# Kernel optimization log

Hardware: AMD Instinct MI355X
Metric: run time of the kernel (lower is better)

The kernel has to match this reference:

```python
import jax, jax.numpy as jnp
import numpy as np

# dims: L=tgt len, S=src len, N=batch, E=embed, H=heads
L, S, N, E, H = 1024, 1024, 4, 1024, 16
HD = E // H  # head dim = 64


def setup_inputs() -> dict:
    key = jax.random.key(0)
    ks = jax.random.split(key, 7)
    w_scale = 0.02
    return {
        "query": jax.random.normal(ks[0], (L, N, E), jnp.float32),
        "key": jax.random.normal(ks[1], (S, N, E), jnp.float32),
        "value": jax.random.normal(ks[2], (S, N, E), jnp.float32),
        "in_proj_weight": jax.random.normal(ks[3], (3 * E, E), jnp.float32) * w_scale,
        "in_proj_bias": jax.random.normal(ks[4], (3 * E,), jnp.float32) * w_scale,
        "out_proj_weight": jax.random.normal(ks[5], (E, E), jnp.float32) * w_scale,
        "out_proj_bias": jax.random.normal(ks[6], (E,), jnp.float32) * w_scale,
    }


def reference(query, key, value, in_proj_weight, in_proj_bias,
              out_proj_weight, out_proj_bias):
    scaling = float(HD) ** -0.5
    # packed QKV projection, sliced exactly as the torch code does
    q = (query @ in_proj_weight[:E].T + in_proj_bias[:E]) * scaling        # (L,N,E)
    k = key @ in_proj_weight[E:2 * E].T + in_proj_bias[E:2 * E]            # (S,N,E)
    v = value @ in_proj_weight[2 * E:].T + in_proj_bias[2 * E:]            # (S,N,E)
    # split heads: (L,N,E) -> (N*H, L, HD)
    q = q.reshape(L, N * H, HD).transpose(1, 0, 2)
    k = k.reshape(S, N * H, HD).transpose(1, 0, 2)
    v = v.reshape(S, N * H, HD).transpose(1, 0, 2)
    scores = jnp.einsum('bld,bsd->bls', q, k)          # (N*H, L, S)
    attn = jax.nn.softmax(scores, axis=-1)
    sig = jax.nn.sigmoid(scores)                        # the need_sigmoid_weights variant
    out = jnp.einsum('bls,bsd->bld', attn, v)          # (N*H, L, HD)
    out = out.transpose(1, 0, 2).reshape(L, N, E)
    out = out @ out_proj_weight.T + out_proj_bias       # (L,N,E)
    # weights averaged over heads, as torch MHA returns: (N,L,S)
    attn_weights = attn.reshape(N, H, L, S).sum(axis=1) / H
    sig_weights = sig.reshape(N, H, L, S).sum(axis=1) / H
    return out, attn_weights, sig_weights
```

## Files before the change

kernel.cpp:

```cpp
#include <hip/hip_runtime.h>

#define L_DIM 1024
#define E_DIM 1024
#define NB 4
#define H_NUM 16
#define HD_DIM 64
#define T_TOK 4096
#define NHB 64

typedef float f32x4 __attribute__((ext_vector_type(4)));
typedef unsigned short u16x8 __attribute__((ext_vector_type(8)));
typedef unsigned short u16x4 __attribute__((ext_vector_type(4)));
typedef __bf16 bf16x8 __attribute__((ext_vector_type(8)));

__device__ inline unsigned short f2bf(float f) {
  unsigned int u = __builtin_bit_cast(unsigned int, f);
  u += 0x7FFFu + ((u >> 16) & 1u);
  return (unsigned short)(u >> 16);
}
__device__ __forceinline__ unsigned int cvt_pk_bf16(float lo, float hi) {
  unsigned int r;
  asm("v_cvt_pk_bf16_f32 %0, %1, %2" : "=v"(r) : "v"(lo), "v"(hi));
  return r;
}
__device__ inline f32x4 mfma16(u16x8 a, u16x8 b, f32x4 c) {
  return __builtin_amdgcn_mfma_f32_16x16x32_bf16(
      __builtin_bit_cast(bf16x8, a), __builtin_bit_cast(bf16x8, b), c, 0, 0, 0);
}

__device__ __forceinline__ void gl2lds16(const void* g, void* l) {
  auto gp = reinterpret_cast<const __attribute__((address_space(1))) unsigned int*>(
      reinterpret_cast<unsigned long long>(g));
  auto lp = reinterpret_cast<__attribute__((address_space(3))) unsigned int*>(
      static_cast<unsigned int>(reinterpret_cast<unsigned long long>(l)));
  __builtin_amdgcn_global_load_lds(gp, lp, 16, 0, 0);
}

__global__ __launch_bounds__(256) void cast_kernel(
    const float* __restrict__ s0, const float* __restrict__ s1,
    const float* __restrict__ s2, const float* __restrict__ s3,
    unsigned short* __restrict__ d0, unsigned short* __restrict__ d1,
    unsigned short* __restrict__ d2, unsigned short* __restrict__ d3,
    int n0, int n1, int n2, int n3) {
  const int y = blockIdx.y;
  const float* s = (y == 0) ? s0 : (y == 1) ? s1 : (y == 2) ? s2 : s3;
  unsigned short* d = (y == 0) ? d0 : (y == 1) ? d1 : (y == 2) ? d2 : d3;
  const int n = (y == 0) ? n0 : (y == 1) ? n1 : (y == 2) ? n2 : n3;
  int idx = (blockIdx.x * 256 + threadIdx.x) * 8;
  const int stride = gridDim.x * 256 * 8;
  for (; idx < n; idx += stride) {
    float4 a = *(const float4*)(s + idx);
    float4 b = *(const float4*)(s + idx + 4);
    u16x8 o = {f2bf(a.x), f2bf(a.y), f2bf(a.z), f2bf(a.w),
               f2bf(b.x), f2bf(b.y), f2bf(b.z), f2bf(b.w)};
    *(u16x8*)(d + idx) = o;
  }
}

__device__ __forceinline__ void stage_tile(const unsigned short* __restrict__ g,
                                           unsigned short* lbuf, int tid) {
  const int r = tid >> 2, c = tid & 3;
  const int sc = c ^ ((r ^ (r >> 2)) & 3);
  gl2lds16(g + (size_t)r * 1024 + sc * 8, lbuf + tid * 8);
  const int r2 = r + 64;
  gl2lds16(g + (size_t)r2 * 1024 + sc * 8, lbuf + (tid + 256) * 8);
}
__device__ __forceinline__ int frag_off(int r, int q) {
  return r * 32 + ((q ^ ((r ^ (r >> 2)) & 3)) << 3);
}

__global__ __launch_bounds__(256) void qkv_gemm(
    const unsigned short* __restrict__ qb, const unsigned short* __restrict__ kb,
    const unsigned short* __restrict__ vb, const unsigned short* __restrict__ Wb,
    const float* __restrict__ bias, unsigned short* __restrict__ q_hm,
    unsigned short* __restrict__ k_hm, unsigned short* __restrict__ v_t) {
  __shared__ __align__(16) unsigned short As[3][4096];
  __shared__ __align__(16) unsigned short Bs[3][4096];
  const int tid = threadIdx.x;
  const int bm = blockIdx.x, bn = blockIdx.y, z = blockIdx.z;
  const unsigned short* Ag = ((z == 0) ? qb : (z == 1) ? kb : vb) + (size_t)bm * 128 * 1024;
  const unsigned short* Bg = Wb + (size_t)z * 1048576 + (size_t)bn * 128 * 1024;
  const float* bc = bias + z * E_DIM;

  const int w = tid >> 6, lane = tid & 63;
  const int wm = w & 1, wn = w >> 1;
  const int quad = lane >> 4, l16 = lane & 15;

  f32x4 acc[4][4];
#pragma unroll
  for (int i = 0; i < 4; i++)
#pragma unroll
    for (int j = 0; j < 4; j++) { f32x4 zz = {0.f, 0.f, 0.f, 0.f}; acc[i][j] = zz; }

  stage_tile(Ag, As[0], tid);
  stage_tile(Bg, Bs[0], tid);

  int cb = 0, sb = 1;
#pragma unroll 1
  for (int kk = 0; kk < 32; kk++) {
    if (kk + 1 < 32) {
      stage_tile(Ag + (kk + 1) * 32, As[sb], tid);
      stage_tile(Bg + (kk + 1) * 32, Bs[sb], tid);
      sb = (sb == 2) ? 0 : sb + 1;
      asm volatile("s_waitcnt vmcnt(4)" ::: "memory");
    } else {
      asm volatile("s_waitcnt vmcnt(0)" ::: "memory");
    }
    __builtin_amdgcn_s_barrier();
    asm volatile("" ::: "memory");
    u16x8 af[4], bfv[4];
#pragma unroll
    for (int mi = 0; mi < 4; mi++) {
      int r = wm * 64 + mi * 16 + l16;
      af[mi] = *(const u16x8*)&As[cb][frag_off(r, quad)];
    }
#pragma unroll
    for (int ni = 0; ni < 4; ni++) {
      int r = wn * 64 + ni * 16 + l16;
      bfv[ni] = *(const u16x8*)&Bs[cb][frag_off(r, quad)];
    }
#pragma unroll
    for (int mi = 0; mi < 4; mi++)
#pragma unroll
      for (int ni = 0; ni < 4; ni++)
        acc[mi][ni] = mfma16(af[mi], bfv[ni], acc[mi][ni]);
    cb = (cb == 2) ? 0 : cb + 1;
  }
#pragma unroll
  for (int ni = 0; ni < 4; ni++) {
    int col = bn * 128 + wn * 64 + ni * 16 + l16;
    float bv = bc[col];
    int h = col >> 6, d = col & 63;
#pragma unroll
    for (int mi = 0; mi < 4; mi++) {
#pragma unroll
      for (int r = 0; r < 4; r++) {
        int t = bm * 128 + wm * 64 + mi * 16 + quad * 4 + r;
        float v = acc[mi][ni][r] + bv;
        int nb = t & 3, pos = t >> 2;
        if (z == 0) {
          v *= 0.125f;
          q_hm[(size_t)((nb * 16 + h) * 1024 + pos) * 64 + d] = f2bf(v);
        } else if (z == 1) {
          k_hm[(size_t)((nb * 16 + h) * 1024 + pos) * 64 + d] = f2bf(v);
        } else {
          v_t[(size_t)((nb * 16 + h) * 64 + d) * 1024 + pos] = f2bf(v);
        }
      }
    }
  }
}

__global__ __launch_bounds__(256, 2) void attn_kernel(
    const unsigned short* __restrict__ q_hm, const unsigned short* __restrict__ k_hm,
    const unsigned short* __restrict__ v_t, unsigned short* __restrict__ o_h,
    float* __restrict__ m_ws, float* __restrict__ r_ws) {
  __shared__ __align__(16) unsigned short stage[6][4096];
  __shared__ __align__(16) unsigned short pt[4][32][68];
  __shared__ float red_m[4][32];
  __shared__ float red_s[4][32];

  const int tid = threadIdx.x;
  const int flat = blockIdx.x + (blockIdx.y << 5);
  const int nf = (flat & 7) * 256 + (flat >> 3);
  const int l0 = (nf & 31) * 32;
  const int b = nf >> 5;
  const int nb = b >> 4, h = b & 15;
  const int w = tid >> 6, lane = tid & 63;
  const int quad = lane >> 4, l16 = lane & 15;

  const int i1 = tid + 256;
  const int r0s = tid >> 3, c0s = tid & 7;
  const int r1s = i1 >> 3, c1s = i1 & 7;
  const int src0 = (c0s ^ (r0s & 7)) * 8;
  const int src1 = (c1s ^ (r1s & 7)) * 8;

  const unsigned short* kbase = k_hm + ((size_t)b << 16);
  const unsigned short* vbase = v_t + ((size_t)b << 16);

  u16x8 bq[2][2];
#pragma unroll
  for (int g = 0; g < 2; g++) {
    const unsigned short* qp =
        q_hm + ((size_t)(b * 1024 + l0 + g * 16 + l16) << 6) + quad * 8;
    bq[g][0] = *(const u16x8*)qp;
    bq[g][1] = *(const u16x8*)(qp + 32);
  }
  asm volatile("" ::: "memory");

  f32x4 acc[16][2];
#pragma unroll
  for (int j = 0; j < 16; j++)
#pragma unroll
    for (int g = 0; g < 2; g++) { f32x4 z = {0.f, 0.f, 0.f, 0.f}; acc[j][g] = z; }

#pragma unroll
  for (int t = 0; t < 4; t++) {
    gl2lds16(kbase + ((size_t)(t * 64 + r0s) << 6) + src0, &stage[t][tid * 8]);
    gl2lds16(kbase + ((size_t)(t * 64 + r1s) << 6) + src1, &stage[t][i1 * 8]);
  }

  const int myrow = w * 16 + l16;
  const int sw0 = ((quad ^ (l16 & 7)) * 8);
  const int sw1 = (((quad + 4) ^ (l16 & 7)) * 8);

#pragma unroll
  for (int i = 0; i < 8; i++) {
    if (i >= 1) {
      const int t0 = 2 * i + 2, t1 = 2 * i + 3;
      if (t0 < 16) {
        gl2lds16(kbase + ((size_t)(t0 * 64 + r0s) << 6) + src0, &stage[t0 % 6][tid * 8]);
        gl2lds16(kbase + ((size_t)(t0 * 64 + r1s) << 6) + src1, &stage[t0 % 6][i1 * 8]);
        gl2lds16(kbase + ((size_t)(t1 * 64 + r0s) << 6) + src0, &stage[t1 % 6][tid * 8]);
        gl2lds16(kbase + ((size_t)(t1 * 64 + r1s) << 6) + src1, &stage[t1 % 6][i1 * 8]);
      } else {
        const int v0 = t0 - 16, v1 = t1 - 16;
        gl2lds16(vbase + ((size_t)r0s << 10) + v0 * 64 + src0, &stage[t0 % 6][tid * 8]);
        gl2lds16(vbase + ((size_t)r1s << 10) + v0 * 64 + src1, &stage[t0 % 6][i1 * 8]);
        gl2lds16(vbase + ((size_t)r0s << 10) + v1 * 64 + src0, &stage[t1 % 6][tid * 8]);
        gl2lds16(vbase + ((size_t)r1s << 10) + v1 * 64 + src1, &stage[t1 % 6][i1 * 8]);
      }
    }
    asm volatile("s_waitcnt vmcnt(4)" ::: "memory");
    __builtin_amdgcn_s_barrier();
    asm volatile("" ::: "memory");
    const int c0 = 2 * i, c1 = 2 * i + 1;
    const unsigned short* kt0 = &stage[c0 % 6][myrow * 64];
    const unsigned short* kt1 = &stage[c1 % 6][myrow * 64];
    u16x8 a00 = *(const u16x8*)(kt0 + sw0);
    u16x8 a01 = *(const u16x8*)(kt0 + sw1);
    u16x8 a10 = *(const u16x8*)(kt1 + sw0);
    u16x8 a11 = *(const u16x8*)(kt1 + sw1);
    acc[c0][0] = mfma16(a00, bq[0][0], acc[c0][0]);
    acc[c0][0] = mfma16(a01, bq[0][1], acc[c0][0]);
    acc[c0][1] = mfma16(a00, bq[1][0], acc[c0][1]);
    acc[c0][1] = mfma16(a01, bq[1][1], acc[c0][1]);
    acc[c1][0] = mfma16(a10, bq[0][0], acc[c1][0]);
    acc[c1][0] = mfma16(a11, bq[0][1], acc[c1][0]);
    acc[c1][1] = mfma16(a10, bq[1][0], acc[c1][1]);
    acc[c1][1] = mfma16(a11, bq[1][1], acc[c1][1]);
  }

  gl2lds16(vbase + ((size_t)r0s << 10) + 2 * 64 + src0, &stage[0][tid * 8]);
  gl2lds16(vbase + ((size_t)r1s << 10) + 2 * 64 + src1, &stage[0][i1 * 8]);
  gl2lds16(vbase + ((size_t)r0s << 10) + 3 * 64 + src0, &stage[1][tid * 8]);
  gl2lds16(vbase + ((size_t)r1s << 10) + 3 * 64 + src1, &stage[1][i1 * 8]);

  float lm0 = -3e38f, lm1 = -3e38f;
#pragma unroll
  for (int j = 0; j < 16; j++)
#pragma unroll
    for (int r = 0; r < 4; r++) {
      lm0 = fmaxf(lm0, acc[j][0][r]);
      lm1 = fmaxf(lm1, acc[j][1][r]);
    }
  lm0 = fmaxf(lm0, __shfl_xor(lm0, 16, 64));
  lm0 = fmaxf(lm0, __shfl_xor(lm0, 32, 64));
  lm1 = fmaxf(lm1, __shfl_xor(lm1, 16, 64));
  lm1 = fmaxf(lm1, __shfl_xor(lm1, 32, 64));
  if (lane < 16) { red_m[w][lane] = lm0; red_m[w][lane + 16] = lm1; }
  asm volatile("s_waitcnt lgkmcnt(0)" ::: "memory");
  __builtin_amdgcn_s_barrier();
  asm volatile("" ::: "memory");
  float m0 = fmaxf(fmaxf(red_m[0][l16], red_m[1][l16]),
                   fmaxf(red_m[2][l16], red_m[3][l16]));
  float m1 = fmaxf(fmaxf(red_m[0][l16 + 16], red_m[1][l16 + 16]),
                   fmaxf(red_m[2][l16 + 16], red_m[3][l16 + 16]));
  float mm = 0.f;
  if (tid < 32)
    mm = fmaxf(fmaxf(red_m[0][tid], red_m[1][tid]),
               fmaxf(red_m[2][tid], red_m[3][tid]));

  float ls0 = 0.f, ls1 = 0.f;
  auto exppk = [&](int t, int slot) {
    float e0a = __expf(acc[t][0][0] - m0), e0b = __expf(acc[t][0][1] - m0);
    float e0c = __expf(acc[t][0][2] - m0), e0d = __expf(acc[t][0][3] - m0);
    float e1a = __expf(acc[t][1][0] - m1), e1b = __expf(acc[t][1][1] - m1);
    float e1c = __expf(acc[t][1][2] - m1), e1d = __expf(acc[t][1][3] - m1);
    ls0 += (e0a + e0b) + (e0c + e0d);
    ls1 += (e1a + e1b) + (e1c + e1d);
    uint2 p0 = {cvt_pk_bf16(e0a, e0b), cvt_pk_bf16(e0c, e0d)};
    uint2 p1 = {cvt_pk_bf16(e1a, e1b), cvt_pk_bf16(e1c, e1d)};
    *(uint2*)&pt[slot][l16][w * 16 + quad * 4] = p0;
    *(uint2*)&pt[slot][16 + l16][w * 16 + quad * 4] = p1;
  };
  exppk(0, 0);
  exppk(1, 1);

  f32x4 oacc0 = {0.f, 0.f, 0.f, 0.f};
  f32x4 oacc1 = {0.f, 0.f, 0.f, 0.f};
#pragma unroll
  for (int i = 0; i < 8; i++) {
    if (i >= 1 && i <= 6) {
      const int v0 = 2 * i + 2, v1 = 2 * i + 3;
      const int b0 = (v0 + 16) % 6, b1 = (v1 + 16) % 6;
      gl2lds16(vbase + ((size_t)r0s << 10) + v0 * 64 + src0, &stage[b0][tid * 8]);
      gl2lds16(vbase + ((size_t)r1s << 10) + v0 * 64 + src1, &stage[b0][i1 * 8]);
      gl2lds16(vbase + ((size_t)r0s << 10) + v1 * 64 + src0, &stage[b1][tid * 8]);
      gl2lds16(vbase + ((size_t)r1s << 10) + v1 * 64 + src1, &stage[b1][i1 * 8]);
    }
    if (i < 7) {
      asm volatile("s_waitcnt vmcnt(4) lgkmcnt(0)" ::: "memory");
    } else {
      asm volatile("s_waitcnt vmcnt(0) lgkmcnt(0)" ::: "memory");
    }
    __builtin_amdgcn_s_barrier();
    asm volatile("" ::: "memory");
    if (i < 7) {
      exppk(2 * i + 2, (2 * i + 2) % 4);
      exppk(2 * i + 3, (2 * i + 3) % 4);
    }
    const int cA = 2 * i, cB = 2 * i + 1;
    const unsigned short* vt0 = &stage[(cA + 16) % 6][myrow * 64];
    const unsigned short* vt1 = &stage[(cB + 16) % 6][myrow * 64];
    u16x8 bvA0 = *(const u16x8*)(vt0 + sw0);
    u16x8 bvA1 = *(const u16x8*)(vt0 + sw1);
    u16x8 bvB0 = *(const u16x8*)(vt1 + sw0);
    u16x8 bvB1 = *(const u16x8*)(vt1 + sw1);
    u16x8 apA00 = *(const u16x8*)&pt[cA % 4][l16][quad * 8];
    u16x8 apA01 = *(const u16x8*)&pt[cA % 4][l16][32 + quad * 8];
    u16x8 apA10 = *(const u16x8*)&pt[cA % 4][16 + l16][quad * 8];
    u16x8 apA11 = *(const u16x8*)&pt[cA % 4][16 + l16][32 + quad * 8];
    u16x8 apB00 = *(const u16x8*)&pt[cB % 4][l16][quad * 8];
    u16x8 apB01 = *(const u16x8*)&pt[cB % 4][l16][32 + quad * 8];
    u16x8 apB10 = *(const u16x8*)&pt[cB % 4][16 + l16][quad * 8];
    u16x8 apB11 = *(const u16x8*)&pt[cB % 4][16 + l16][32 + quad * 8];
    oacc0 = mfma16(apA00, bvA0, oacc0);
    oacc0 = mfma16(apA01, bvA1, oacc0);
    oacc0 = mfma16(apB00, bvB0, oacc0);
    oacc0 = mfma16(apB01, bvB1, oacc0);
    oacc1 = mfma16(apA10, bvA0, oacc1);
    oacc1 = mfma16(apA11, bvA1, oacc1);
    oacc1 = mfma16(apB10, bvB0, oacc1);
    oacc1 = mfma16(apB11, bvB1, oacc1);
  }

  ls0 += __shfl_xor(ls0, 16, 64);
  ls0 += __shfl_xor(ls0, 32, 64);
  ls1 += __shfl_xor(ls1, 16, 64);
  ls1 += __shfl_xor(ls1, 32, 64);
  if (lane < 16) { red_s[w][lane] = ls0; red_s[w][lane + 16] = ls1; }
  asm volatile("s_waitcnt lgkmcnt(0)" ::: "memory");
  __builtin_amdgcn_s_barrier();
  asm volatile("" ::: "memory");
  float rv0 = 1.0f / (red_s[0][l16] + red_s[1][l16] + red_s[2][l16] + red_s[3][l16]);
  float rv1 = 1.0f / (red_s[0][l16 + 16] + red_s[1][l16 + 16] +
                      red_s[2][l16 + 16] + red_s[3][l16 + 16]);
  if (tid < 32) {
    float ssv = red_s[0][tid] + red_s[1][tid] + red_s[2][tid] + red_s[3][tid];
    m_ws[b * 1024 + l0 + tid] = mm;
    r_ws[b * 1024 + l0 + tid] = 1.0f / ssv;
  }

#pragma unroll
  for (int r = 0; r < 4; r++) {
    int lr = quad * 4 + r;
    float rr0 = __shfl(rv0, lr, 64);
    float rr1 = __shfl(rv1, lr, 64);
    int t0 = (l0 + lr) * 4 + nb;
    int t1 = (l0 + 16 + lr) * 4 + nb;
    o_h[((size_t)t0 << 10) + h * 64 + w * 16 + l16] = f2bf(oacc0[r] * rr0);
    o_h[((size_t)t1 << 10) + h * 64 + w * 16 + l16] = f2bf(oacc1[r] * rr1);
  }
}

__global__ __launch_bounds__(256, 2) void weights_kernel(
    const unsigned short* __restrict__ q_hm, const unsigned short* __restrict__ k_hm,
    const float* __restrict__ m_ws, const float* __restrict__ r_ws,
    float* __restrict__ attn_out, float* __restrict__ sig_out) {
  __shared__ __align__(16) unsigned short qs[4][4096];
  __shared__ __align__(16) unsigned short ks[4][4096];
  __shared__ float ml[16][64];
  __shared__ float rl[16][64];
  __shared__ float cl[16][64];

  const int tid = threadIdx.x;
  const int flat = blockIdx.x + (blockIdx.y << 4) + (blockIdx.z << 8);
  const int xcd = flat & 7, local = flat >> 3;
  const int nb = xcd >> 1;
  const int idx2 = ((xcd & 1) << 7) + local;
  const int l0 = (idx2 >> 4) << 6;
  const int s0 = (idx2 & 15) << 6;

  const int w = tid >> 6, lane = tid & 63;
  const int quad = lane >> 4, l16 = lane & 15;

  const int i1 = tid + 256;
  const int r0s = tid >> 3, c0s = tid & 7;
  const int r1s = i1 >> 3, c1s = i1 & 7;
  const int src0 = (c0s ^ (r0s & 7)) * 8;
  const int src1 = (c1s ^ (r1s & 7)) * 8;

  {
    int idx = tid * 4;
    int hh = idx >> 6, ii = idx & 63;
    int bb = nb * 16 + hh;
    float4 mv4 = *(const float4*)&m_ws[bb * 1024 + l0 + ii];
    float4 rv4 = *(const float4*)&r_ws[bb * 1024 + l0 + ii];
    *(float4*)&ml[hh][ii] = mv4;
    *(float4*)&rl[hh][ii] = rv4;
    float4 cv4 = {__expf(-mv4.x), __expf(-mv4.y), __expf(-mv4.z), __expf(-mv4.w)};
    *(float4*)&cl[hh][ii] = cv4;
  }

  const int sw0 = ((quad ^ (l16 & 7)) * 8);
  const int sw1 = (((quad + 4) ^ (l16 & 7)) * 8);

  auto stageQK = [&](int h) {
    const int bb = nb * 16 + h;
    const unsigned short* qb = q_hm + ((size_t)(bb * 1024 + l0) << 6);
    const unsigned short* kb = k_hm + ((size_t)(bb * 1024 + s0) << 6);
    const int bf = h & 3;
    gl2lds16(qb + (r0s << 6) + src0, &qs[bf][tid * 8]);
    gl2lds16(qb + (r1s << 6) + src1, &qs[bf][i1 * 8]);
    gl2lds16(kb + (r0s << 6) + src0, &ks[bf][tid * 8]);
    gl2lds16(kb + (r1s << 6) + src1, &ks[bf][i1 * 8]);
  };

  f32x4 accA[4], accS[4];
#pragma unroll
  for (int i = 0; i < 4; i++) {
    f32x4 zz = {0.f, 0.f, 0.f, 0.f};
    accA[i] = zz; accS[i] = zz;
  }

  stageQK(0);
  stageQK(1);

  auto computeH = [&](int h) {
    const int bf = h & 3;
    const unsigned short* qt = &qs[bf][(w * 16 + l16) * 64];
    u16x8 a0 = *(const u16x8*)(qt + sw0);
    u16x8 a1 = *(const u16x8*)(qt + sw1);
    f32x4 mv = *(const f32x4*)&ml[h][w * 16 + quad * 4];
    f32x4 rv = *(const f32x4*)&rl[h][w * 16 + quad * 4];
    f32x4 cv = *(const f32x4*)&cl[h][w * 16 + quad * 4];
#pragma unroll
    for (int ni = 0; ni < 4; ni++) {
      const unsigned short* kt = &ks[bf][(ni * 16 + l16) * 64];
      u16x8 b0 = *(const u16x8*)(kt + sw0);
      u16x8 b1 = *(const u16x8*)(kt + sw1);
      f32x4 scv = {0.f, 0.f, 0.f, 0.f};
      scv = mfma16(a0, b0, scv);
      scv = mfma16(a1, b1, scv);
#pragma unroll
      for (int r = 0; r < 4; r++) {
        float e = __expf(scv[r] - mv[r]);
        accA[ni][r] += e * rv[r];
        accS[ni][r] += e * __builtin_amdgcn_rcpf(e + cv[r]);
      }
    }
  };

#pragma unroll 1
  for (int p = 0; p < 8; ++p) {
    asm volatile("s_waitcnt vmcnt(0) lgkmcnt(0)" ::: "memory");
    __builtin_amdgcn_s_barrier();
    asm volatile("" ::: "memory");
    if (p < 7) {
      stageQK(2 * p + 2);
      stageQK(2 * p + 3);
    }
    computeH(2 * p);
    computeH(2 * p + 1);
  }

  const float inv_h = 1.0f / 16.0f;
  const int lrow0 = l0 + w * 16;
#pragma unroll
  for (int ni = 0; ni < 4; ni++) {
#pragma unroll
    for (int r = 0; r < 4; r++) {
      int l = lrow0 + quad * 4 + r;
      int s = s0 + ni * 16 + l16;
      size_t idx = ((size_t)nb * 1024 + l) * 1024 + s;
      attn_out[idx] = accA[ni][r] * inv_h;
      sig_out[idx] = accS[ni][r] * inv_h;
    }
  }
}

__global__ __launch_bounds__(256) void out_gemm(
    const unsigned short* __restrict__ o_h, const unsigned short* __restrict__ Wb,
    const float* __restrict__ bias, float* __restrict__ out) {
  __shared__ __align__(16) unsigned short As[3][4096];
  __shared__ __align__(16) unsigned short Bs[3][4096];
  const int tid = threadIdx.x;
  const int bm = blockIdx.x, bn = blockIdx.y;
  const unsigned short* Ag = o_h + (size_t)bm * 128 * 1024;
  const unsigned short* Bg = Wb + (size_t)bn * 128 * 1024;

  const int w = tid >> 6, lane = tid & 63;
  const int wm = w & 1, wn = w >> 1;
  const int quad = lane >> 4, l16 = lane & 15;

  f32x4 acc[4][4];
#pragma unroll
  for (int i = 0; i < 4; i++)
#pragma unroll
    for (int j = 0; j < 4; j++) { f32x4 zz = {0.f, 0.f, 0.f, 0.f}; acc[i][j] = zz; }

  stage_tile(Ag, As[0], tid);
  stage_tile(Bg, Bs[0], tid);

  int cb = 0, sb = 1;
#pragma unroll 1
  for (int kk = 0; kk < 32; kk++) {
    if (kk + 1 < 32) {
      stage_tile(Ag + (kk + 1) * 32, As[sb], tid);
      stage_tile(Bg + (kk + 1) * 32, Bs[sb], tid);
      sb = (sb == 2) ? 0 : sb + 1;
      asm volatile("s_waitcnt vmcnt(4)" ::: "memory");
    } else {
      asm volatile("s_waitcnt vmcnt(0)" ::: "memory");
    }
    __builtin_amdgcn_s_barrier();
    asm volatile("" ::: "memory");
    u16x8 af[4], bfv[4];
#pragma unroll
    for (int mi = 0; mi < 4; mi++) {
      int r = wm * 64 + mi * 16 + l16;
      af[mi] = *(const u16x8*)&As[cb][frag_off(r, quad)];
    }
#pragma unroll
    for (int ni = 0; ni < 4; ni++) {
      int r = wn * 64 + ni * 16 + l16;
      bfv[ni] = *(const u16x8*)&Bs[cb][frag_off(r, quad)];
    }
#pragma unroll
    for (int mi = 0; mi < 4; mi++)
#pragma unroll
      for (int ni = 0; ni < 4; ni++)
        acc[mi][ni] = mfma16(af[mi], bfv[ni], acc[mi][ni]);
    cb = (cb == 2) ? 0 : cb + 1;
  }
#pragma unroll
  for (int ni = 0; ni < 4; ni++) {
    int col = bn * 128 + wn * 64 + ni * 16 + l16;
    float bv = bias[col];
#pragma unroll
    for (int mi = 0; mi < 4; mi++) {
#pragma unroll
      for (int r = 0; r < 4; r++) {
        int t = bm * 128 + wm * 64 + mi * 16 + quad * 4 + r;
        out[(size_t)t * E_DIM + col] = acc[mi][ni][r] + bv;
      }
    }
  }
}

extern "C" void kernel_launch(void* const* d_in, const int* in_sizes, int n_in,
                              void* d_out, int out_size, void* d_ws, size_t ws_size,
                              hipStream_t stream) {
  const float* qin  = (const float*)d_in[0];
  const float* kin  = (const float*)d_in[1];
  const float* vin  = (const float*)d_in[2];
  const float* Wqkv = (const float*)d_in[3];
  const float* bqkv = (const float*)d_in[4];
  const float* Wout = (const float*)d_in[5];
  const float* bout = (const float*)d_in[6];
  float* out      = (float*)d_out;
  float* attn_out = out + 4194304;
  float* sig_out  = out + 8388608;

  unsigned short* q_hm = (unsigned short*)d_ws;
  unsigned short* k_hm = q_hm + 4194304;
  unsigned short* v_t  = q_hm + 8388608;
  unsigned short* o_h  = q_hm + 12582912;
  float* m_ws = (float*)(q_hm + 16777216);
  float* r_ws = m_ws + 65536;

  unsigned short* qb = (unsigned short*)(out + 4194304);
  unsigned short* kb = qb + 4194304;
  unsigned short* vb = qb + 8388608;
  unsigned short* Wqkvb = o_h;
  unsigned short* Woutb = v_t;

  cast_kernel<<<dim3(2048, 4), 256, 0, stream>>>(
      qin, kin, vin, Wqkv, qb, kb, vb, Wqkvb,
      4194304, 4194304, 4194304, 3145728);
  qkv_gemm<<<dim3(32, 8, 3), 256, 0, stream>>>(qb, kb, vb, Wqkvb, bqkv,
                                               q_hm, k_hm, v_t);
  attn_kernel<<<dim3(32, 64), 256, 0, stream>>>(q_hm, k_hm, v_t, o_h, m_ws, r_ws);
  cast_kernel<<<dim3(512, 1), 256, 0, stream>>>(
      Wout, Wout, Wout, Wout, Woutb, Woutb, Woutb, Woutb,
      1048576, 0, 0, 0);
  weights_kernel<<<dim3(16, 16, 4), 256, 0, stream>>>(q_hm, k_hm, m_ws, r_ws,
                                                      attn_out, sig_out);
  out_gemm<<<dim3(32, 8), 256, 0, stream>>>(o_h, Woutb, bout, out);
}
```

Measured before the change: 250.4 us.

## Split attention work across 8 waves and pipeline weights kernel per head

The attention kernel moves from 256 to 512 threads. Each wave now owns one 16-row group of queries against a 16-column slice, so each thread holds half the accumulators and issues half the loads. Softmax normalisation now finishes before the PV loop, and exponentials are computed in place. Separately, the weights kernel's loop is restructured to stage one head ahead at a time with partial vmcnt waits instead of a full drain every two heads. The larger blocks cut register pressure per thread and add occupancy, at the cost of more barrier participants and smaller MFMA work per wave.

```diff
diff --git a/kernel.cpp b/kernel.cpp
--- a/kernel.cpp
+++ b/kernel.cpp
@@ -151,14 +151,14 @@
   }
 }
 
-__global__ __launch_bounds__(256, 2) void attn_kernel(
+__global__ __launch_bounds__(512, 4) void attn_kernel(
     const unsigned short* __restrict__ q_hm, const unsigned short* __restrict__ k_hm,
     const unsigned short* __restrict__ v_t, unsigned short* __restrict__ o_h,
     float* __restrict__ m_ws, float* __restrict__ r_ws) {
   __shared__ __align__(16) unsigned short stage[6][4096];
   __shared__ __align__(16) unsigned short pt[4][32][68];
-  __shared__ float red_m[4][32];
-  __shared__ float red_s[4][32];
+  __shared__ float red_m[8][16];
+  __shared__ float red_s[8][16];
 
   const int tid = threadIdx.x;
   const int flat = blockIdx.x + (blockIdx.y << 5);
@@ -167,40 +167,33 @@
   const int b = nf >> 5;
   const int nb = b >> 4, h = b & 15;
   const int w = tid >> 6, lane = tid & 63;
+  const int sgrp = w & 3, lgrp = w >> 2;
   const int quad = lane >> 4, l16 = lane & 15;
 
-  const int i1 = tid + 256;
   const int r0s = tid >> 3, c0s = tid & 7;
-  const int r1s = i1 >> 3, c1s = i1 & 7;
   const int src0 = (c0s ^ (r0s & 7)) * 8;
-  const int src1 = (c1s ^ (r1s & 7)) * 8;
 
   const unsigned short* kbase = k_hm + ((size_t)b << 16);
   const unsigned short* vbase = v_t + ((size_t)b << 16);
 
-  u16x8 bq[2][2];
-#pragma unroll
-  for (int g = 0; g < 2; g++) {
+  u16x8 bq0, bq1;
+  {
     const unsigned short* qp =
-        q_hm + ((size_t)(b * 1024 + l0 + g * 16 + l16) << 6) + quad * 8;
-    bq[g][0] = *(const u16x8*)qp;
-    bq[g][1] = *(const u16x8*)(qp + 32);
+        q_hm + ((size_t)(b * 1024 + l0 + lgrp * 16 + l16) << 6) + quad * 8;
+    bq0 = *(const u16x8*)qp;
+    bq1 = *(const u16x8*)(qp + 32);
   }
   asm volatile("" ::: "memory");
 
-  f32x4 acc[16][2];
-#pragma unroll
-  for (int j = 0; j < 16; j++)
-#pragma unroll
-    for (int g = 0; g < 2; g++) { f32x4 z = {0.f, 0.f, 0.f, 0.f}; acc[j][g] = z; }
-
-#pragma unroll
-  for (int t = 0; t < 4; t++) {
+  f32x4 acc[16];
+#pragma unroll
+  for (int j = 0; j < 16; j++) { f32x4 z = {0.f, 0.f, 0.f, 0.f}; acc[j] = z; }
+
+#pragma unroll
+  for (int t = 0; t < 4; t++)
     gl2lds16(kbase + ((size_t)(t * 64 + r0s) << 6) + src0, &stage[t][tid * 8]);
-    gl2lds16(kbase + ((size_t)(t * 64 + r1s) << 6) + src1, &stage[t][i1 * 8]);
-  }
-
-  const int myrow = w * 16 + l16;
+
+  const int arow = sgrp * 16 + l16;
   const int sw0 = ((quad ^ (l16 & 7)) * 8);
   const int sw1 = (((quad + 4) ^ (l16 & 7)) * 8);
 
@@ -210,157 +203,128 @@
       const int t0 = 2 * i + 2, t1 = 2 * i + 3;
       if (t0 < 16) {
         gl2lds16(kbase + ((size_t)(t0 * 64 + r0s) << 6) + src0, &stage[t0 % 6][tid * 8]);
-        gl2lds16(kbase + ((size_t)(t0 * 64 + r1s) << 6) + src1, &stage[t0 % 6][i1 * 8]);
         gl2lds16(kbase + ((size_t)(t1 * 64 + r0s) << 6) + src0, &stage[t1 % 6][tid * 8]);
-        gl2lds16(kbase + ((size_t)(t1 * 64 + r1s) << 6) + src1, &stage[t1 % 6][i1 * 8]);
       } else {
         const int v0 = t0 - 16, v1 = t1 - 16;
         gl2lds16(vbase + ((size_t)r0s << 10) + v0 * 64 + src0, &stage[t0 % 6][tid * 8]);
-        gl2lds16(vbase + ((size_t)r1s << 10) + v0 * 64 + src1, &stage[t0 % 6][i1 * 8]);
         gl2lds16(vbase + ((size_t)r0s << 10) + v1 * 64 + src0, &stage[t1 % 6][tid * 8]);
-        gl2lds16(vbase + ((size_t)r1s << 10) + v1 * 64 + src1, &stage[t1 % 6][i1 * 8]);
       }
     }
-    asm volatile("s_waitcnt vmcnt(4)" ::: "memory");
+    asm volatile("s_waitcnt vmcnt(2)" ::: "memory");
     __builtin_amdgcn_s_barrier();
     asm volatile("" ::: "memory");
     const int c0 = 2 * i, c1 = 2 * i + 1;
-    const unsigned short* kt0 = &stage[c0 % 6][myrow * 64];
-    const unsigned short* kt1 = &stage[c1 % 6][myrow * 64];
+    const unsigned short* kt0 = &stage[c0 % 6][arow * 64];
+    const unsigned short* kt1 = &stage[c1 % 6][arow * 64];
     u16x8 a00 = *(const u16x8*)(kt0 + sw0);
     u16x8 a01 = *(const u16x8*)(kt0 + sw1);
     u16x8 a10 = *(const u16x8*)(kt1 + sw0);
     u16x8 a11 = *(const u16x8*)(kt1 + sw1);
-    acc[c0][0] = mfma16(a00, bq[0][0], acc[c0][0]);
-    acc[c0][0] = mfma16(a01, bq[0][1], acc[c0][0]);
-    acc[c0][1] = mfma16(a00, bq[1][0], acc[c0][1]);
-    acc[c0][1] = mfma16(a01, bq[1][1], acc[c0][1]);
-    acc[c1][0] = mfma16(a10, bq[0][0], acc[c1][0]);
-    acc[c1][0] = mfma16(a11, bq[0][1], acc[c1][0]);
-    acc[c1][1] = mfma16(a10, bq[1][0], acc[c1][1]);
-    acc[c1][1] = mfma16(a11, bq[1][1], acc[c1][1]);
+    acc[c0] = mfma16(a00, bq0, acc[c0]);
+    acc[c0] = mfma16(a01, bq1, acc[c0]);
+    acc[c1] = mfma16(a10, bq0, acc[c1]);
+    acc[c1] = mfma16(a11, bq1, acc[c1]);
   }
 
   gl2lds16(vbase + ((size_t)r0s << 10) + 2 * 64 + src0, &stage[0][tid * 8]);
-  gl2lds16(vbase + ((size_t)r1s << 10) + 2 * 64 + src1, &stage[0][i1 * 8]);
   gl2lds16(vbase + ((size_t)r0s << 10) + 3 * 64 + src0, &stage[1][tid * 8]);
-  gl2lds16(vbase + ((size_t)r1s << 10) + 3 * 64 + src1, &stage[1][i1 * 8]);
-
-  float lm0 = -3e38f, lm1 = -3e38f;
+
+  float lm = -3e38f;
 #pragma unroll
   for (int j = 0; j < 16; j++)
 #pragma unroll
-    for (int r = 0; r < 4; r++) {
-      lm0 = fmaxf(lm0, acc[j][0][r]);
-      lm1 = fmaxf(lm1, acc[j][1][r]);
-    }
-  lm0 = fmaxf(lm0, __shfl_xor(lm0, 16, 64));
-  lm0 = fmaxf(lm0, __shfl_xor(lm0, 32, 64));
-  lm1 = fmaxf(lm1, __shfl_xor(lm1, 16, 64));
-  lm1 = fmaxf(lm1, __shfl_xor(lm1, 32, 64));
-  if (lane < 16) { red_m[w][lane] = lm0; red_m[w][lane + 16] = lm1; }
+    for (int r = 0; r < 4; r++) lm = fmaxf(lm, acc[j][r]);
+  lm = fmaxf(lm, __shfl_xor(lm, 16, 64));
+  lm = fmaxf(lm, __shfl_xor(lm, 32, 64));
+  if (lane < 16) red_m[w][lane] = lm;
   asm volatile("s_waitcnt lgkmcnt(0)" ::: "memory");
   __builtin_amdgcn_s_barrier();
   asm volatile("" ::: "memory");
-  float m0 = fmaxf(fmaxf(red_m[0][l16], red_m[1][l16]),
-                   fmaxf(red_m[2][l16], red_m[3][l16]));
-  float m1 = fmaxf(fmaxf(red_m[0][l16 + 16], red_m[1][l16 + 16]),
-                   fmaxf(red_m[2][l16 + 16], red_m[3][l16 + 16]));
+  const int rbase = lgrp * 4;
+  float m = fmaxf(fmaxf(red_m[rbase][l16], red_m[rbase + 1][l16]),
+                  fmaxf(red_m[rbase + 2][l16], red_m[rbase + 3][l16]));
   float mm = 0.f;
-  if (tid < 32)
-    mm = fmaxf(fmaxf(red_m[0][tid], red_m[1][tid]),
-               fmaxf(red_m[2][tid], red_m[3][tid]));
-
-  float ls0 = 0.f, ls1 = 0.f;
-  auto exppk = [&](int t, int slot) {
-    float e0a = __expf(acc[t][0][0] - m0), e0b = __expf(acc[t][0][1] - m0);
-    float e0c = __expf(acc[t][0][2] - m0), e0d = __expf(acc[t][0][3] - m0);
-    float e1a = __expf(acc[t][1][0] - m1), e1b = __expf(acc[t][1][1] - m1);
-    float e1c = __expf(acc[t][1][2] - m1), e1d = __expf(acc[t][1][3] - m1);
-    ls0 += (e0a + e0b) + (e0c + e0d);
-    ls1 += (e1a + e1b) + (e1c + e1d);
-    uint2 p0 = {cvt_pk_bf16(e0a, e0b), cvt_pk_bf16(e0c, e0d)};
-    uint2 p1 = {cvt_pk_bf16(e1a, e1b), cvt_pk_bf16(e1c, e1d)};
-    *(uint2*)&pt[slot][l16][w * 16 + quad * 4] = p0;
-    *(uint2*)&pt[slot][16 + l16][w * 16 + quad * 4] = p1;
+  if (tid < 32) {
+    int g4 = (tid >> 4) * 4, li = tid & 15;
+    mm = fmaxf(fmaxf(red_m[g4][li], red_m[g4 + 1][li]),
+               fmaxf(red_m[g4 + 2][li], red_m[g4 + 3][li]));
+  }
+
+  float ls = 0.f;
+#pragma unroll
+  for (int j = 0; j < 16; j++) {
+#pragma unroll
+    for (int r = 0; r < 4; r++) {
+      float e = __expf(acc[j][r] - m);
+      acc[j][r] = e;
+      ls += e;
+    }
+  }
+  ls += __shfl_xor(ls, 16, 64);
+  ls += __shfl_xor(ls, 32, 64);
+  if (lane < 16) red_s[w][lane] = ls;
+  asm volatile("s_waitcnt lgkmcnt(0)" ::: "memory");
+  __builtin_amdgcn_s_barrier();
+  asm volatile("" ::: "memory");
+  float rv = 1.0f / (red_s[rbase][l16] + red_s[rbase + 1][l16] +
+                     red_s[rbase + 2][l16] + red_s[rbase + 3][l16]);
+  if (tid < 32) {
+    int g4 = (tid >> 4) * 4, li = tid & 15;
+    float ssv = red_s[g4][li] + red_s[g4 + 1][li] + red_s[g4 + 2][li] + red_s[g4 + 3][li];
+    m_ws[b * 1024 + l0 + tid] = mm;
+    r_ws[b * 1024 + l0 + tid] = 1.0f / ssv;
+  }
+
+  auto ptwrite = [&](int t, int slot) {
+    uint2 p = {cvt_pk_bf16(acc[t][0], acc[t][1]), cvt_pk_bf16(acc[t][2], acc[t][3])};
+    *(uint2*)&pt[slot][lgrp * 16 + l16][sgrp * 16 + quad * 4] = p;
   };
-  exppk(0, 0);
-  exppk(1, 1);
-
-  f32x4 oacc0 = {0.f, 0.f, 0.f, 0.f};
-  f32x4 oacc1 = {0.f, 0.f, 0.f, 0.f};
+  ptwrite(0, 0);
+  ptwrite(1, 1);
+
+  f32x4 oacc = {0.f, 0.f, 0.f, 0.f};
+  const int vrow = sgrp * 16 + l16;
 #pragma unroll
   for (int i = 0; i < 8; i++) {
     if (i >= 1 && i <= 6) {
       const int v0 = 2 * i + 2, v1 = 2 * i + 3;
-      const int b0 = (v0 + 16) % 6, b1 = (v1 + 16) % 6;
-      gl2lds16(vbase + ((size_t)r0s << 10) + v0 * 64 + src0, &stage[b0][tid * 8]);
-      gl2lds16(vbase + ((size_t)r1s << 10) + v0 * 64 + src1, &stage[b0][i1 * 8]);
-      gl2lds16(vbase + ((size_t)r0s << 10) + v1 * 64 + src0, &stage[b1][tid * 8]);
-      gl2lds16(vbase + ((size_t)r1s << 10) + v1 * 64 + src1, &stage[b1][i1 * 8]);
+      gl2lds16(vbase + ((size_t)r0s << 10) + v0 * 64 + src0, &stage[(v0 + 16) % 6][tid * 8]);
+      gl2lds16(vbase + ((size_t)r0s << 10) + v1 * 64 + src0, &stage[(v1 + 16) % 6][tid * 8]);
     }
     if (i < 7) {
-      asm volatile("s_waitcnt vmcnt(4) lgkmcnt(0)" ::: "memory");
+      asm volatile("s_waitcnt vmcnt(2) lgkmcnt(0)" ::: "memory");
     } else {
       asm volatile("s_waitcnt vmcnt(0) lgkmcnt(0)" ::: "memory");
     }
     __builtin_amdgcn_s_barrier();
     asm volatile("" ::: "memory");
     if (i < 7) {
-      exppk(2 * i + 2, (2 * i + 2) % 4);
-      exppk(2 * i + 3, (2 * i + 3) % 4);
+      ptwrite(2 * i + 2, (2 * i + 2) % 4);
+      ptwrite(2 * i + 3, (2 * i + 3) % 4);
     }
     const int cA = 2 * i, cB = 2 * i + 1;
-    const unsigned short* vt0 = &stage[(cA + 16) % 6][myrow * 64];
-    const unsigned short* vt1 = &stage[(cB + 16) % 6][myrow * 64];
+    const unsigned short* vt0 = &stage[(cA + 16) % 6][vrow * 64];
+    const unsigned short* vt1 = &stage[(cB + 16) % 6][vrow * 64];
     u16x8 bvA0 = *(const u16x8*)(vt0 + sw0);
     u16x8 bvA1 = *(const u16x8*)(vt0 + sw1);
     u16x8 bvB0 = *(const u16x8*)(vt1 + sw0);
     u16x8 bvB1 = *(const u16x8*)(vt1 + sw1);
-    u16x8 apA00 = *(const u16x8*)&pt[cA % 4][l16][quad * 8];
-    u16x8 apA01 = *(const u16x8*)&pt[cA % 4][l16][32 + quad * 8];
-    u16x8 apA10 = *(const u16x8*)&pt[cA % 4][16 + l16][quad * 8];
-    u16x8 apA11 = *(const u16x8*)&pt[cA % 4][16 + l16][32 + quad * 8];
-    u16x8 apB00 = *(const u16x8*)&pt[cB % 4][l16][quad * 8];
-    u16x8 apB01 = *(const u16x8*)&pt[cB % 4][l16][32 + quad * 8];
-    u16x8 apB10 = *(const u16x8*)&pt[cB % 4][16 + l16][quad * 8];
-    u16x8 apB11 = *(const u16x8*)&pt[cB % 4][16 + l16][32 + quad * 8];
-    oacc0 = mfma16(apA00, bvA0, oacc0);
-    oacc0 = mfma16(apA01, bvA1, oacc0);
-    oacc0 = mfma16(apB00, bvB0, oacc0);
-    oacc0 = mfma16(apB01, bvB1, oacc0);
-    oacc1 = mfma16(apA10, bvA0, oacc1);
-    oacc1 = mfma16(apA11, bvA1, oacc1);
-    oacc1 = mfma16(apB10, bvB0, oacc1);
-    oacc1 = mfma16(apB11, bvB1, oacc1);
-  }
-
-  ls0 += __shfl_xor(ls0, 16, 64);
-  ls0 += __shfl_xor(ls0, 32, 64);
-  ls1 += __shfl_xor(ls1, 16, 64);
-  ls1 += __shfl_xor(ls1, 32, 64);
-  if (lane < 16) { red_s[w][lane] = ls0; red_s[w][lane + 16] = ls1; }
-  asm volatile("s_waitcnt lgkmcnt(0)" ::: "memory");
-  __builtin_amdgcn_s_barrier();
-  asm volatile("" ::: "memory");
-  float rv0 = 1.0f / (red_s[0][l16] + red_s[1][l16] + red_s[2][l16] + red_s[3][l16]);
-  float rv1 = 1.0f / (red_s[0][l16 + 16] + red_s[1][l16 + 16] +
-                      red_s[2][l16 + 16] + red_s[3][l16 + 16]);
-  if (tid < 32) {
-    float ssv = red_s[0][tid] + red_s[1][tid] + red_s[2][tid] + red_s[3][tid];
-    m_ws[b * 1024 + l0 + tid] = mm;
-    r_ws[b * 1024 + l0 + tid] = 1.0f / ssv;
+    u16x8 apA0 = *(const u16x8*)&pt[cA % 4][lgrp * 16 + l16][quad * 8];
+    u16x8 apA1 = *(const u16x8*)&pt[cA % 4][lgrp * 16 + l16][32 + quad * 8];
+    u16x8 apB0 = *(const u16x8*)&pt[cB % 4][lgrp * 16 + l16][quad * 8];
+    u16x8 apB1 = *(const u16x8*)&pt[cB % 4][lgrp * 16 + l16][32 + quad * 8];
+    oacc = mfma16(apA0, bvA0, oacc);
+    oacc = mfma16(apA1, bvA1, oacc);
+    oacc = mfma16(apB0, bvB0, oacc);
+    oacc = mfma16(apB1, bvB1, oacc);
   }
 
 #pragma unroll
   for (int r = 0; r < 4; r++) {
     int lr = quad * 4 + r;
-    float rr0 = __shfl(rv0, lr, 64);
-    float rr1 = __shfl(rv1, lr, 64);
-    int t0 = (l0 + lr) * 4 + nb;
-    int t1 = (l0 + 16 + lr) * 4 + nb;
-    o_h[((size_t)t0 << 10) + h * 64 + w * 16 + l16] = f2bf(oacc0[r] * rr0);
-    o_h[((size_t)t1 << 10) + h * 64 + w * 16 + l16] = f2bf(oacc1[r] * rr1);
+    float rr = __shfl(rv, lr, 64);
+    int t = (l0 + lgrp * 16 + lr) * 4 + nb;
+    o_h[((size_t)t << 10) + h * 64 + sgrp * 16 + l16] = f2bf(oacc[r] * rr);
   }
 }
 
@@ -426,6 +390,7 @@
 
   stageQK(0);
   stageQK(1);
+  asm volatile("s_waitcnt lgkmcnt(0)" ::: "memory");
 
   auto computeH = [&](int h) {
     const int bf = h & 3;
@@ -453,17 +418,21 @@
   };
 
 #pragma unroll 1
-  for (int p = 0; p < 8; ++p) {
-    asm volatile("s_waitcnt vmcnt(0) lgkmcnt(0)" ::: "memory");
+  for (int h = 0; h < 14; ++h) {
+    stageQK(h + 2);
+    asm volatile("s_waitcnt vmcnt(8)" ::: "memory");
     __builtin_amdgcn_s_barrier();
     asm volatile("" ::: "memory");
-    if (p < 7) {
-      stageQK(2 * p + 2);
-      stageQK(2 * p + 3);
-    }
-    computeH(2 * p);
-    computeH(2 * p + 1);
-  }
+    computeH(h);
+  }
+  asm volatile("s_waitcnt vmcnt(4)" ::: "memory");
+  __builtin_amdgcn_s_barrier();
+  asm volatile("" ::: "memory");
+  computeH(14);
+  asm volatile("s_waitcnt vmcnt(0)" ::: "memory");
+  __builtin_amdgcn_s_barrier();
+  asm volatile("" ::: "memory");
+  computeH(15);
 
   const float inv_h = 1.0f / 16.0f;
   const int lrow0 = l0 + w * 16;
@@ -581,7 +550,7 @@
       4194304, 4194304, 4194304, 3145728);
   qkv_gemm<<<dim3(32, 8, 3), 256, 0, stream>>>(qb, kb, vb, Wqkvb, bqkv,
                                                q_hm, k_hm, v_t);
-  attn_kernel<<<dim3(32, 64), 256, 0, stream>>>(q_hm, k_hm, v_t, o_h, m_ws, r_ws);
+  attn_kernel<<<dim3(32, 64), 512, 0, stream>>>(q_hm, k_hm, v_t, o_h, m_ws, r_ws);
   cast_kernel<<<dim3(512, 1), 256, 0, stream>>>(
       Wout, Wout, Wout, Wout, Woutb, Woutb, Woutb, Woutb,
       1048576, 0, 0, 0);
```

Result: no change. 254.7 us (+1.7%).

## Deepen weights-kernel QK prefetch pipeline and fold Wout cast into first cast launch

Applied to the files above, without the earlier changes.

The weights kernel now stages one head ahead per iteration and waits only with partial vmcnt counts, instead of doing two heads per phase behind a full vmcnt(0)/lgkmcnt(0) drain. This uses the 4-slot LDS ring to overlap global-to-LDS loads with MFMA and exp work. The out-projection weight cast moves into the first cast launch as a fifth grid row, which removes one kernel launch. Its bf16 buffer now lives in the attn_out scratch area, so out_gemm is moved ahead of weights_kernel so it reads the buffer before that region is overwritten.

```diff
diff --git a/kernel.cpp b/kernel.cpp
--- a/kernel.cpp
+++ b/kernel.cpp
@@ -39,13 +39,15 @@
 __global__ __launch_bounds__(256) void cast_kernel(
     const float* __restrict__ s0, const float* __restrict__ s1,
     const float* __restrict__ s2, const float* __restrict__ s3,
+    const float* __restrict__ s4,
     unsigned short* __restrict__ d0, unsigned short* __restrict__ d1,
     unsigned short* __restrict__ d2, unsigned short* __restrict__ d3,
-    int n0, int n1, int n2, int n3) {
+    unsigned short* __restrict__ d4,
+    int n0, int n1, int n2, int n3, int n4) {
   const int y = blockIdx.y;
-  const float* s = (y == 0) ? s0 : (y == 1) ? s1 : (y == 2) ? s2 : s3;
-  unsigned short* d = (y == 0) ? d0 : (y == 1) ? d1 : (y == 2) ? d2 : d3;
-  const int n = (y == 0) ? n0 : (y == 1) ? n1 : (y == 2) ? n2 : n3;
+  const float* s = (y == 0) ? s0 : (y == 1) ? s1 : (y == 2) ? s2 : (y == 3) ? s3 : s4;
+  unsigned short* d = (y == 0) ? d0 : (y == 1) ? d1 : (y == 2) ? d2 : (y == 3) ? d3 : d4;
+  const int n = (y == 0) ? n0 : (y == 1) ? n1 : (y == 2) ? n2 : (y == 3) ? n3 : n4;
   int idx = (blockIdx.x * 256 + threadIdx.x) * 8;
   const int stride = gridDim.x * 256 * 8;
   for (; idx < n; idx += stride) {
@@ -426,6 +428,7 @@
 
   stageQK(0);
   stageQK(1);
+  asm volatile("s_waitcnt lgkmcnt(0)" ::: "memory");
 
   auto computeH = [&](int h) {
     const int bf = h & 3;
@@ -453,17 +456,21 @@
   };
 
 #pragma unroll 1
-  for (int p = 0; p < 8; ++p) {
-    asm volatile("s_waitcnt vmcnt(0) lgkmcnt(0)" ::: "memory");
+  for (int h = 0; h < 14; ++h) {
+    stageQK(h + 2);
+    asm volatile("s_waitcnt vmcnt(8)" ::: "memory");
     __builtin_amdgcn_s_barrier();
     asm volatile("" ::: "memory");
-    if (p < 7) {
-      stageQK(2 * p + 2);
-      stageQK(2 * p + 3);
-    }
-    computeH(2 * p);
-    computeH(2 * p + 1);
-  }
+    computeH(h);
+  }
+  asm volatile("s_waitcnt vmcnt(4)" ::: "memory");
+  __builtin_amdgcn_s_barrier();
+  asm volatile("" ::: "memory");
+  computeH(14);
+  asm volatile("s_waitcnt vmcnt(0)" ::: "memory");
+  __builtin_amdgcn_s_barrier();
+  asm volatile("" ::: "memory");
+  computeH(15);
 
   const float inv_h = 1.0f / 16.0f;
   const int lrow0 = l0 + w * 16;
@@ -574,18 +581,15 @@
   unsigned short* kb = qb + 4194304;
   unsigned short* vb = qb + 8388608;
   unsigned short* Wqkvb = o_h;
-  unsigned short* Woutb = v_t;
-
-  cast_kernel<<<dim3(2048, 4), 256, 0, stream>>>(
-      qin, kin, vin, Wqkv, qb, kb, vb, Wqkvb,
-      4194304, 4194304, 4194304, 3145728);
+  unsigned short* Woutb = qb + 12582912;
+
+  cast_kernel<<<dim3(2048, 5), 256, 0, stream>>>(
+      qin, kin, vin, Wqkv, Wout, qb, kb, vb, Wqkvb, Woutb,
+      4194304, 4194304, 4194304, 3145728, 1048576);
   qkv_gemm<<<dim3(32, 8, 3), 256, 0, stream>>>(qb, kb, vb, Wqkvb, bqkv,
                                                q_hm, k_hm, v_t);
   attn_kernel<<<dim3(32, 64), 256, 0, stream>>>(q_hm, k_hm, v_t, o_h, m_ws, r_ws);
-  cast_kernel<<<dim3(512, 1), 256, 0, stream>>>(
-      Wout, Wout, Wout, Wout, Woutb, Woutb, Woutb, Woutb,
-      1048576, 0, 0, 0);
+  out_gemm<<<dim3(32, 8), 256, 0, stream>>>(o_h, Woutb, bout, out);
   weights_kernel<<<dim3(16, 16, 4), 256, 0, stream>>>(q_hm, k_hm, m_ws, r_ws,
                                                       attn_out, sig_out);
-  out_gemm<<<dim3(32, 8), 256, 0, stream>>>(o_h, Woutb, bout, out);
-}
+}
```

Result: no change. 248.2 us (-0.9%).
